# Performance work log

Measured on AMD Instinct MI355X. Metric: run time of the kernel, lower is better.

Reference implementation:

```python
import jax, jax.numpy as jnp
import numpy as np

N_OBJ = 4096      # n_objects (fixed node count; fc1 consumes flattened node features)
F_IN = 256        # in_feats
H = 256           # n_hidden
C = 128           # n_classes
NE = 8            # number of edge types
EPT = 131072      # edges per etype (avg in-degree 32)


def setup_inputs() -> dict:
    key = jax.random.key(0)
    ks = jax.random.split(key, 16)
    s = 0.02  # weight init scale
    inp = {
        "feat": jax.random.normal(ks[0], (N_OBJ, F_IN), dtype=jnp.float32),
        "edges": jax.random.randint(ks[1], (NE, 2, EPT), 0, N_OBJ, dtype=jnp.int64),
        # 3 hetero layers: layer0 (F_IN->H), layers 1,2 (H->H), each with per-etype Linear
        "W0": jax.random.normal(ks[2], (NE, H, F_IN), dtype=jnp.float32) * s,
        "b0": jnp.zeros((NE, H), dtype=jnp.float32),
        "W1": jax.random.normal(ks[3], (NE, H, H), dtype=jnp.float32) * s,
        "b1": jnp.zeros((NE, H), dtype=jnp.float32),
        "W2": jax.random.normal(ks[4], (NE, H, H), dtype=jnp.float32) * s,
        "b2": jnp.zeros((NE, H), dtype=jnp.float32),
        "fc1_w": jax.random.normal(ks[5], (H, N_OBJ * H), dtype=jnp.float32) * 0.002,
        "fc1_b": jnp.zeros((H,), dtype=jnp.float32),
        "fc2_w": jax.random.normal(ks[6], (C, H), dtype=jnp.float32) * s,
        "fc2_b": jnp.zeros((C,), dtype=jnp.float32),
    }
    return inp


def _hetero_layer(h, W, b, edges):
    # Per-etype linear: Wh[e] = h @ W[e].T + b[e]   -> [NE, N, H]
    Wh = jnp.einsum('nf,ehf->enh', h, W) + b[:, None, :]

    def per_etype(wh, src, dst):
        msg = wh[src]                                            # gather: [EPT, H]
        ssum = jax.ops.segment_sum(msg, dst, num_segments=N_OBJ)  # [N, H]
        deg = jax.ops.segment_sum(jnp.ones_like(dst, dtype=wh.dtype), dst,
                                  num_segments=N_OBJ)             # [N]
        return ssum / jnp.maximum(deg, 1.0)[:, None]              # mean reduce

    agg = jax.vmap(per_etype)(Wh, edges[:, 0], edges[:, 1])  # [NE, N, H]
    # multi_update_all cross-type aggregator 'sum', then activation (relu)
    return jax.nn.relu(agg.sum(axis=0))


def reference(feat, edges, W0, b0, W1, b1, W2, b2, fc1_w, fc1_b, fc2_w, fc2_b):
    h = _hetero_layer(feat, W0, b0, edges)
    h = _hetero_layer(h, W1, b1, edges)
    h = _hetero_layer(h, W2, b2, edges)
    flat = h.reshape(-1)                          # [N*H]
    z = jax.nn.relu(fc1_w @ flat + fc1_b)         # [H]
    out = jax.nn.sigmoid(fc2_w @ z + fc2_b)       # [C]
    return out
```

## Files before the change

### kernel.cpp

```cpp
#include <hip/hip_runtime.h>
#include <math.h>

#define N_OBJ 4096
#define F     256
#define NE    8
#define EPT   131072
#define KCAT  (NE * F)
#define C_OUT 128
#define FC1_K (N_OBJ * F)
#define CHUNK 32768
#define NCH   (FC1_K / CHUNK)
#define RPB   8

typedef __attribute__((ext_vector_type(8))) short s8v;
typedef __attribute__((ext_vector_type(4))) float f4v;

__device__ inline float bf2f(unsigned short u) {
    unsigned int x = ((unsigned int)u) << 16;
    return __builtin_bit_cast(float, x);
}
__device__ inline unsigned short f2bf(float f) {
    unsigned int x = __builtin_bit_cast(unsigned int, f);
    x += 0x7fff + ((x >> 16) & 1);
    return (unsigned short)(x >> 16);
}


__global__ __launch_bounds__(256) void k_count_deg(const int* __restrict__ edges,
                                                   int* __restrict__ deg) {
    int gid = blockIdx.x * 256 + threadIdx.x;
    int e = gid >> 17;
    int i = gid & (EPT - 1);
    int dst = edges[(e * 2 + 1) * EPT + i];
    atomicAdd(&deg[e * N_OBJ + dst], 1);
}

__global__ __launch_bounds__(256) void k_scan(const int* __restrict__ deg,
                                              int* __restrict__ rowptr,
                                              int* __restrict__ cursor,
                                              float* __restrict__ invdeg) {
    int e = blockIdx.x;
    int t = threadIdx.x;
    __shared__ int part[256];
    int local[16];
    int base = e * N_OBJ + t * 16;
    int s = 0;
#pragma unroll
    for (int i = 0; i < 16; ++i) { local[i] = deg[base + i]; s += local[i]; }
    part[t] = s;
    __syncthreads();
    for (int off = 1; off < 256; off <<= 1) {
        int v = (t >= off) ? part[t - off] : 0;
        __syncthreads();
        part[t] += v;
        __syncthreads();
    }
    int run = part[t] - s;
#pragma unroll
    for (int i = 0; i < 16; ++i) {
        rowptr[base + i] = run;
        cursor[base + i] = run;
        invdeg[base + i] = 1.0f / fmaxf((float)local[i], 1.0f);
        run += local[i];
    }
}

__global__ __launch_bounds__(256) void k_fill(const int* __restrict__ edges,
                                              int* __restrict__ cursor,
                                              int* __restrict__ col) {
    int gid = blockIdx.x * 256 + threadIdx.x;
    int e = gid >> 17;
    int i = gid & (EPT - 1);
    int src = edges[(e * 2 + 0) * EPT + i];
    int dst = edges[(e * 2 + 1) * EPT + i];
    int pos = atomicAdd(&cursor[e * N_OBJ + dst], 1);
    col[e * EPT + pos] = src;
}

__global__ __launch_bounds__(256) void k_bmask(const int* __restrict__ deg,
                                               unsigned int* __restrict__ bmask) {
    int n = blockIdx.x * 256 + threadIdx.x;
    unsigned int m = 0;
#pragma unroll
    for (int e = 0; e < NE; ++e) m |= (deg[e * N_OBJ + n] > 0) ? (1u << e) : 0u;
    bmask[n] = m;
}

__global__ __launch_bounds__(256) void k_cvt(const float* __restrict__ s,
                                             unsigned short* __restrict__ d, int n4) {
    int i = blockIdx.x * 256 + threadIdx.x;
    if (i < n4) {
        float4 v = ((const float4*)s)[i];
        ushort4 o;
        o.x = f2bf(v.x); o.y = f2bf(v.y); o.z = f2bf(v.z); o.w = f2bf(v.w);
        ((ushort4*)d)[i] = o;
    }
}

__global__ __launch_bounds__(256) void k_aggregate(const unsigned short* __restrict__ h_in,
                                                   const int* __restrict__ rowptr,
                                                   const int* __restrict__ deg,
                                                   const int* __restrict__ col,
                                                   const float* __restrict__ invdeg,
                                                   unsigned short* __restrict__ ah) {
    int wid = blockIdx.x * 4 + (threadIdx.x >> 6);
    int lane = threadIdx.x & 63;
    int e = wid >> 12;
    int n = wid & (N_OBJ - 1);
    int beg = rowptr[wid];
    int cnt = deg[wid];
    const int* cl = col + e * EPT + beg;
    const ushort4* h4 = (const ushort4*)h_in;
    float a0 = 0.f, a1 = 0.f, a2 = 0.f, a3 = 0.f;
    int k = 0;
    for (; k + 8 <= cnt; k += 8) {
        int s0 = cl[k],     s1 = cl[k + 1], s2 = cl[k + 2], s3 = cl[k + 3];
        int s4 = cl[k + 4], s5 = cl[k + 5], s6 = cl[k + 6], s7 = cl[k + 7];
        ushort4 v0 = h4[s0 * 64 + lane];
        ushort4 v1 = h4[s1 * 64 + lane];
        ushort4 v2 = h4[s2 * 64 + lane];
        ushort4 v3 = h4[s3 * 64 + lane];
        ushort4 v4 = h4[s4 * 64 + lane];
        ushort4 v5 = h4[s5 * 64 + lane];
        ushort4 v6 = h4[s6 * 64 + lane];
        ushort4 v7 = h4[s7 * 64 + lane];
        a0 += bf2f(v0.x) + bf2f(v1.x) + bf2f(v2.x) + bf2f(v3.x)
            + bf2f(v4.x) + bf2f(v5.x) + bf2f(v6.x) + bf2f(v7.x);
        a1 += bf2f(v0.y) + bf2f(v1.y) + bf2f(v2.y) + bf2f(v3.y)
            + bf2f(v4.y) + bf2f(v5.y) + bf2f(v6.y) + bf2f(v7.y);
        a2 += bf2f(v0.z) + bf2f(v1.z) + bf2f(v2.z) + bf2f(v3.z)
            + bf2f(v4.z) + bf2f(v5.z) + bf2f(v6.z) + bf2f(v7.z);
        a3 += bf2f(v0.w) + bf2f(v1.w) + bf2f(v2.w) + bf2f(v3.w)
            + bf2f(v4.w) + bf2f(v5.w) + bf2f(v6.w) + bf2f(v7.w);
    }
    for (; k < cnt; ++k) {
        ushort4 v = h4[cl[k] * 64 + lane];
        a0 += bf2f(v.x); a1 += bf2f(v.y); a2 += bf2f(v.z); a3 += bf2f(v.w);
    }
    float sc = invdeg[wid];
    ushort4 o;
    o.x = f2bf(a0 * sc); o.y = f2bf(a1 * sc); o.z = f2bf(a2 * sc); o.w = f2bf(a3 * sc);
    ((ushort4*)ah)[n * (KCAT / 4) + e * (F / 4) + lane] = o;
}

template <int OUTBF>
__global__ __launch_bounds__(256) void k_gemm(const unsigned short* __restrict__ A,
                                              const unsigned short* __restrict__ Wb,
                                              const float* __restrict__ bias,
                                              const unsigned int* __restrict__ bmask,
                                              void* __restrict__ Cout) {
    __shared__ short As[64][40];
    __shared__ short Bs[64][40];
    int m0 = blockIdx.x * 64, n0 = blockIdx.y * 64;
    int t = threadIdx.x;
    int wave = t >> 6, lane = t & 63;
    int srow = t >> 2, sseg = t & 3;
    int r = lane & 15, g = lane >> 4;
    f4v acc[4];
#pragma unroll
    for (int i = 0; i < 4; ++i) acc[i] = (f4v){0.f, 0.f, 0.f, 0.f};
    const short* Ap = (const short*)A;
    const short* Wp = (const short*)Wb;
    for (int k0 = 0; k0 < KCAT; k0 += 32) {
        int e = k0 >> 8, f0 = k0 & 255;
        s8v va = *(const s8v*)(Ap + (size_t)(m0 + srow) * KCAT + k0 + sseg * 8);
        s8v vb = *(const s8v*)(Wp + (size_t)e * F * F + (size_t)(n0 + srow) * F + f0 + sseg * 8);
        __syncthreads();
        *(s8v*)&As[srow][sseg * 8] = va;
        *(s8v*)&Bs[srow][sseg * 8] = vb;
        __syncthreads();
        s8v bfrag = *(const s8v*)&Bs[wave * 16 + r][g * 8];
#pragma unroll
        for (int mf = 0; mf < 4; ++mf) {
            s8v afrag = *(const s8v*)&As[mf * 16 + r][g * 8];
            acc[mf] = __builtin_amdgcn_mfma_f32_16x16x32_bf16(afrag, bfrag, acc[mf], 0, 0, 0);
        }
    }
    int coln = n0 + wave * 16 + r;
    float bcol[NE];
#pragma unroll
    for (int e = 0; e < NE; ++e) bcol[e] = bias[e * F + coln];
#pragma unroll
    for (int mf = 0; mf < 4; ++mf) {
#pragma unroll
        for (int reg = 0; reg < 4; ++reg) {
            int m = m0 + mf * 16 + g * 4 + reg;
            unsigned int msk = bmask[m];
            float v = acc[mf][reg];
#pragma unroll
            for (int e = 0; e < NE; ++e)
                if ((msk >> e) & 1) v += bcol[e];
            v = fmaxf(v, 0.f);
            if (OUTBF) ((unsigned short*)Cout)[(size_t)m * F + coln] = f2bf(v);
            else       ((float*)Cout)[(size_t)m * F + coln] = v;
        }
    }
}

__global__ __launch_bounds__(256) void k_fc1(const float* __restrict__ Wf,
                                             const float* __restrict__ flat,
                                             float* __restrict__ zpart) {
    int c = blockIdx.x;
    int jg = blockIdx.y;
    int t = threadIdx.x;
    const float4* fp = (const float4*)(flat + (size_t)c * CHUNK);
    size_t base = (size_t)(jg * RPB) * FC1_K + (size_t)c * CHUNK;
    float acc[RPB] = {};
#pragma unroll 2
    for (int it = 0; it < CHUNK / 4 / 256; ++it) {
        int q = it * 256 + t;
        float4 x4 = fp[q];
#pragma unroll
        for (int rr = 0; rr < RPB; ++rr) {
            float4 w4 = *(const float4*)(Wf + base + (size_t)rr * FC1_K + (size_t)q * 4);
            acc[rr] = fmaf(w4.x, x4.x,
                      fmaf(w4.y, x4.y,
                      fmaf(w4.z, x4.z,
                      fmaf(w4.w, x4.w, acc[rr]))));
        }
    }
    __shared__ float red[4][RPB];
    int lane = t & 63, wv = t >> 6;
#pragma unroll
    for (int rr = 0; rr < RPB; ++rr) {
        float s = acc[rr];
#pragma unroll
        for (int off = 32; off > 0; off >>= 1) s += __shfl_down(s, off, 64);
        if (lane == 0) red[wv][rr] = s;
    }
    __syncthreads();
    if (t < RPB) {
        float s = red[0][t] + red[1][t] + red[2][t] + red[3][t];
        zpart[c * 256 + jg * RPB + t] = s;
    }
}

__global__ __launch_bounds__(256) void k_final(const float* __restrict__ zpart,
                                               const float* __restrict__ fc1_b,
                                               const float* __restrict__ fc2_w,
                                               const float* __restrict__ fc2_b,
                                               float* __restrict__ out) {
    __shared__ float z[256];
    int t = threadIdx.x;
    float s = fc1_b[t];
#pragma unroll
    for (int c = 0; c < NCH; ++c) s += zpart[c * 256 + t];
    z[t] = fmaxf(s, 0.0f);
    __syncthreads();
    if (t < C_OUT) {
        float acc = fc2_b[t];
        for (int k = 0; k < 256; ++k) acc = fmaf(fc2_w[t * 256 + k], z[k], acc);
        out[t] = 1.0f / (1.0f + expf(-acc));
    }
}

extern "C" void kernel_launch(void* const* d_in, const int* in_sizes, int n_in,
                              void* d_out, int out_size, void* d_ws, size_t ws_size,
                              hipStream_t stream) {
    const float* feat  = (const float*)d_in[0];
    const int*   edges = (const int*)d_in[1];
    const float* W0    = (const float*)d_in[2];
    const float* b0    = (const float*)d_in[3];
    const float* W1    = (const float*)d_in[4];
    const float* b1    = (const float*)d_in[5];
    const float* W2    = (const float*)d_in[6];
    const float* b2    = (const float*)d_in[7];
    const float* fc1_w = (const float*)d_in[8];
    const float* fc1_b = (const float*)d_in[9];
    const float* fc2_w = (const float*)d_in[10];
    const float* fc2_b = (const float*)d_in[11];
    float* out = (float*)d_out;

    char* ws = (char*)d_ws;
    size_t off = 0;
    auto alloc = [&](size_t bytes) {
        void* p = ws + off;
        off = (off + bytes + 255) & ~(size_t)255;
        return p;
    };
    int*            deg    = (int*)            alloc(NE * N_OBJ * 4);
    int*            rowptr = (int*)            alloc(NE * N_OBJ * 4);
    int*            cursor = (int*)            alloc(NE * N_OBJ * 4);
    float*          invdeg = (float*)          alloc(NE * N_OBJ * 4);
    int*            col    = (int*)            alloc(NE * EPT * 4);
    unsigned int*   bmask  = (unsigned int*)   alloc(N_OBJ * 4);
    float*          zpart  = (float*)          alloc(NCH * 256 * 4);
    unsigned short* Wb0    = (unsigned short*) alloc((size_t)NE * F * F * 2);
    unsigned short* Wb1    = (unsigned short*) alloc((size_t)NE * F * F * 2);
    unsigned short* Wb2    = (unsigned short*) alloc((size_t)NE * F * F * 2);
    unsigned short* featb  = (unsigned short*) alloc((size_t)N_OBJ * F * 2);
    unsigned short* h_ba   = (unsigned short*) alloc((size_t)N_OBJ * F * 2);
    unsigned short* h_bb   = (unsigned short*) alloc((size_t)N_OBJ * F * 2);
    float*          h_f32  = (float*)          alloc((size_t)N_OBJ * F * 4);
    unsigned short* ah     = (unsigned short*) alloc((size_t)N_OBJ * KCAT * 2);
    (void)ws_size; (void)in_sizes; (void)n_in; (void)out_size;

    hipMemsetAsync(deg, 0, NE * N_OBJ * 4, stream);
    k_count_deg<<<NE * EPT / 256, 256, 0, stream>>>(edges, deg);
    k_scan<<<NE, 256, 0, stream>>>(deg, rowptr, cursor, invdeg);
    k_fill<<<NE * EPT / 256, 256, 0, stream>>>(edges, cursor, col);
    k_bmask<<<N_OBJ / 256, 256, 0, stream>>>(deg, bmask);
    k_cvt<<<512, 256, 0, stream>>>(W0, Wb0, NE * F * F / 4);
    k_cvt<<<512, 256, 0, stream>>>(W1, Wb1, NE * F * F / 4);
    k_cvt<<<512, 256, 0, stream>>>(W2, Wb2, NE * F * F / 4);
    k_cvt<<<1024, 256, 0, stream>>>(feat, featb, N_OBJ * F / 4);

    dim3 ggrid(N_OBJ / 64, F / 64);
    int agrid = NE * N_OBJ / 4;

    k_aggregate<<<agrid, 256, 0, stream>>>(featb, rowptr, deg, col, invdeg, ah);
    k_gemm<1><<<ggrid, 256, 0, stream>>>(ah, Wb0, b0, bmask, h_ba);
    k_aggregate<<<agrid, 256, 0, stream>>>(h_ba, rowptr, deg, col, invdeg, ah);
    k_gemm<1><<<ggrid, 256, 0, stream>>>(ah, Wb1, b1, bmask, h_bb);
    k_aggregate<<<agrid, 256, 0, stream>>>(h_bb, rowptr, deg, col, invdeg, ah);
    k_gemm<0><<<ggrid, 256, 0, stream>>>(ah, Wb2, b2, bmask, h_f32);

    dim3 fgrid(NCH, 256 / RPB);
    k_fc1<<<fgrid, 256, 0, stream>>>(fc1_w, h_f32, zpart);
    k_final<<<1, 256, 0, stream>>>(zpart, fc1_b, fc2_w, fc2_b, out);
}
```

Before: 522.9 us.

## Retile GEMM to 32x64 blocks, restructure fc1 per-row, merge conversion kernels

After: 522.2 us. Within noise of the previous version (-0.1%).

```diff
diff --git a/kernel.cpp b/kernel.cpp
--- a/kernel.cpp
+++ b/kernel.cpp
@@ -8,9 +8,6 @@
 #define KCAT  (NE * F)
 #define C_OUT 128
 #define FC1_K (N_OBJ * F)
-#define CHUNK 32768
-#define NCH   (FC1_K / CHUNK)
-#define RPB   8
 
 typedef __attribute__((ext_vector_type(8))) short s8v;
 typedef __attribute__((ext_vector_type(4))) float f4v;
@@ -86,15 +83,28 @@
     bmask[n] = m;
 }
 
-__global__ __launch_bounds__(256) void k_cvt(const float* __restrict__ s,
-                                             unsigned short* __restrict__ d, int n4) {
+#define WQ4 (NE * F * F / 4)
+#define FQ4 (N_OBJ * F / 4)
+__global__ __launch_bounds__(256) void k_cvt_all(const float* __restrict__ W0,
+                                                 const float* __restrict__ W1,
+                                                 const float* __restrict__ W2,
+                                                 const float* __restrict__ feat,
+                                                 unsigned short* __restrict__ Wb0,
+                                                 unsigned short* __restrict__ Wb1,
+                                                 unsigned short* __restrict__ Wb2,
+                                                 unsigned short* __restrict__ featb) {
     int i = blockIdx.x * 256 + threadIdx.x;
-    if (i < n4) {
-        float4 v = ((const float4*)s)[i];
-        ushort4 o;
-        o.x = f2bf(v.x); o.y = f2bf(v.y); o.z = f2bf(v.z); o.w = f2bf(v.w);
-        ((ushort4*)d)[i] = o;
-    }
+    const float* s;
+    unsigned short* d;
+    int j;
+    if (i < WQ4)            { s = W0;   d = Wb0;   j = i; }
+    else if (i < 2 * WQ4)   { s = W1;   d = Wb1;   j = i - WQ4; }
+    else if (i < 3 * WQ4)   { s = W2;   d = Wb2;   j = i - 2 * WQ4; }
+    else                    { s = feat; d = featb; j = i - 3 * WQ4; }
+    float4 v = ((const float4*)s)[j];
+    ushort4 o;
+    o.x = f2bf(v.x); o.y = f2bf(v.y); o.z = f2bf(v.z); o.w = f2bf(v.w);
+    ((ushort4*)d)[j] = o;
 }
 
 __global__ __launch_bounds__(256) void k_aggregate(const unsigned short* __restrict__ h_in,
@@ -144,55 +154,66 @@
 }
 
 template <int OUTBF>
-__global__ __launch_bounds__(256) void k_gemm(const unsigned short* __restrict__ A,
+__global__ __launch_bounds__(128) void k_gemm(const unsigned short* __restrict__ A,
                                               const unsigned short* __restrict__ Wb,
                                               const float* __restrict__ bias,
                                               const unsigned int* __restrict__ bmask,
                                               void* __restrict__ Cout) {
-    __shared__ short As[64][40];
+    __shared__ short As[32][40];
     __shared__ short Bs[64][40];
-    int m0 = blockIdx.x * 64, n0 = blockIdx.y * 64;
+    int m0 = blockIdx.x * 32, n0 = blockIdx.y * 64;
     int t = threadIdx.x;
     int wave = t >> 6, lane = t & 63;
-    int srow = t >> 2, sseg = t & 3;
     int r = lane & 15, g = lane >> 4;
-    f4v acc[4];
-#pragma unroll
-    for (int i = 0; i < 4; ++i) acc[i] = (f4v){0.f, 0.f, 0.f, 0.f};
+    int arow = t >> 2, aseg = t & 3;
+    int brow = t >> 1, bseg = (t & 1) * 2;
+    f4v acc[2][2];
+#pragma unroll
+    for (int i = 0; i < 2; ++i)
+#pragma unroll
+        for (int j = 0; j < 2; ++j) acc[i][j] = (f4v){0.f, 0.f, 0.f, 0.f};
     const short* Ap = (const short*)A;
     const short* Wp = (const short*)Wb;
     for (int k0 = 0; k0 < KCAT; k0 += 32) {
         int e = k0 >> 8, f0 = k0 & 255;
-        s8v va = *(const s8v*)(Ap + (size_t)(m0 + srow) * KCAT + k0 + sseg * 8);
-        s8v vb = *(const s8v*)(Wp + (size_t)e * F * F + (size_t)(n0 + srow) * F + f0 + sseg * 8);
+        s8v va = *(const s8v*)(Ap + (size_t)(m0 + arow) * KCAT + k0 + aseg * 8);
+        const short* wbase = Wp + (size_t)e * F * F + (size_t)(n0 + brow) * F + f0;
+        s8v vb0 = *(const s8v*)(wbase + bseg * 8);
+        s8v vb1 = *(const s8v*)(wbase + bseg * 8 + 8);
         __syncthreads();
-        *(s8v*)&As[srow][sseg * 8] = va;
-        *(s8v*)&Bs[srow][sseg * 8] = vb;
+        *(s8v*)&As[arow][aseg * 8] = va;
+        *(s8v*)&Bs[brow][bseg * 8] = vb0;
+        *(s8v*)&Bs[brow][bseg * 8 + 8] = vb1;
         __syncthreads();
-        s8v bfrag = *(const s8v*)&Bs[wave * 16 + r][g * 8];
-#pragma unroll
-        for (int mf = 0; mf < 4; ++mf) {
-            s8v afrag = *(const s8v*)&As[mf * 16 + r][g * 8];
-            acc[mf] = __builtin_amdgcn_mfma_f32_16x16x32_bf16(afrag, bfrag, acc[mf], 0, 0, 0);
+        s8v bf0 = *(const s8v*)&Bs[wave * 32 + r][g * 8];
+        s8v bf1 = *(const s8v*)&Bs[wave * 32 + 16 + r][g * 8];
+#pragma unroll
+        for (int m = 0; m < 2; ++m) {
+            s8v af = *(const s8v*)&As[m * 16 + r][g * 8];
+            acc[m][0] = __builtin_amdgcn_mfma_f32_16x16x32_bf16(af, bf0, acc[m][0], 0, 0, 0);
+            acc[m][1] = __builtin_amdgcn_mfma_f32_16x16x32_bf16(af, bf1, acc[m][1], 0, 0, 0);
         }
     }
-    int coln = n0 + wave * 16 + r;
-    float bcol[NE];
-#pragma unroll
-    for (int e = 0; e < NE; ++e) bcol[e] = bias[e * F + coln];
-#pragma unroll
-    for (int mf = 0; mf < 4; ++mf) {
-#pragma unroll
-        for (int reg = 0; reg < 4; ++reg) {
-            int m = m0 + mf * 16 + g * 4 + reg;
-            unsigned int msk = bmask[m];
-            float v = acc[mf][reg];
-#pragma unroll
-            for (int e = 0; e < NE; ++e)
-                if ((msk >> e) & 1) v += bcol[e];
-            v = fmaxf(v, 0.f);
-            if (OUTBF) ((unsigned short*)Cout)[(size_t)m * F + coln] = f2bf(v);
-            else       ((float*)Cout)[(size_t)m * F + coln] = v;
+#pragma unroll
+    for (int nn = 0; nn < 2; ++nn) {
+        int coln = n0 + wave * 32 + nn * 16 + r;
+        float bcol[NE];
+#pragma unroll
+        for (int e = 0; e < NE; ++e) bcol[e] = bias[e * F + coln];
+#pragma unroll
+        for (int m = 0; m < 2; ++m) {
+#pragma unroll
+            for (int reg = 0; reg < 4; ++reg) {
+                int mm = m0 + m * 16 + g * 4 + reg;
+                unsigned int msk = bmask[mm];
+                float v = acc[m][nn][reg];
+#pragma unroll
+                for (int e = 0; e < NE; ++e)
+                    if ((msk >> e) & 1) v += bcol[e];
+                v = fmaxf(v, 0.f);
+                if (OUTBF) ((unsigned short*)Cout)[(size_t)mm * F + coln] = f2bf(v);
+                else       ((float*)Cout)[(size_t)mm * F + coln] = v;
+            }
         }
     }
 }
@@ -201,38 +222,27 @@
                                              const float* __restrict__ flat,
                                              float* __restrict__ zpart) {
     int c = blockIdx.x;
-    int jg = blockIdx.y;
+    int j = blockIdx.y;
     int t = threadIdx.x;
-    const float4* fp = (const float4*)(flat + (size_t)c * CHUNK);
-    size_t base = (size_t)(jg * RPB) * FC1_K + (size_t)c * CHUNK;
-    float acc[RPB] = {};
-#pragma unroll 2
-    for (int it = 0; it < CHUNK / 4 / 256; ++it) {
+    const float4* wp = (const float4*)(Wf + (size_t)j * FC1_K + (size_t)c * 65536);
+    const float4* fp = (const float4*)(flat + (size_t)c * 65536);
+    float s = 0.0f;
+#pragma unroll 8
+    for (int it = 0; it < 64; ++it) {
         int q = it * 256 + t;
+        float4 w4 = wp[q];
         float4 x4 = fp[q];
-#pragma unroll
-        for (int rr = 0; rr < RPB; ++rr) {
-            float4 w4 = *(const float4*)(Wf + base + (size_t)rr * FC1_K + (size_t)q * 4);
-            acc[rr] = fmaf(w4.x, x4.x,
-                      fmaf(w4.y, x4.y,
-                      fmaf(w4.z, x4.z,
-                      fmaf(w4.w, x4.w, acc[rr]))));
-        }
-    }
-    __shared__ float red[4][RPB];
-    int lane = t & 63, wv = t >> 6;
-#pragma unroll
-    for (int rr = 0; rr < RPB; ++rr) {
-        float s = acc[rr];
-#pragma unroll
-        for (int off = 32; off > 0; off >>= 1) s += __shfl_down(s, off, 64);
-        if (lane == 0) red[wv][rr] = s;
-    }
+        s = fmaf(w4.x, x4.x, s);
+        s = fmaf(w4.y, x4.y, s);
+        s = fmaf(w4.z, x4.z, s);
+        s = fmaf(w4.w, x4.w, s);
+    }
+#pragma unroll
+    for (int off = 32; off > 0; off >>= 1) s += __shfl_down(s, off, 64);
+    __shared__ float red[4];
+    if ((t & 63) == 0) red[t >> 6] = s;
     __syncthreads();
-    if (t < RPB) {
-        float s = red[0][t] + red[1][t] + red[2][t] + red[3][t];
-        zpart[c * 256 + jg * RPB + t] = s;
-    }
+    if (t == 0) zpart[c * 256 + j] = red[0] + red[1] + red[2] + red[3];
 }
 
 __global__ __launch_bounds__(256) void k_final(const float* __restrict__ zpart,
@@ -244,7 +254,7 @@
     int t = threadIdx.x;
     float s = fc1_b[t];
 #pragma unroll
-    for (int c = 0; c < NCH; ++c) s += zpart[c * 256 + t];
+    for (int c = 0; c < 16; ++c) s += zpart[c * 256 + t];
     z[t] = fmaxf(s, 0.0f);
     __syncthreads();
     if (t < C_OUT) {
@@ -284,7 +294,7 @@
     float*          invdeg = (float*)          alloc(NE * N_OBJ * 4);
     int*            col    = (int*)            alloc(NE * EPT * 4);
     unsigned int*   bmask  = (unsigned int*)   alloc(N_OBJ * 4);
-    float*          zpart  = (float*)          alloc(NCH * 256 * 4);
+    float*          zpart  = (float*)          alloc(16 * 256 * 4);
     unsigned short* Wb0    = (unsigned short*) alloc((size_t)NE * F * F * 2);
     unsigned short* Wb1    = (unsigned short*) alloc((size_t)NE * F * F * 2);
     unsigned short* Wb2    = (unsigned short*) alloc((size_t)NE * F * F * 2);
@@ -300,22 +310,20 @@
     k_scan<<<NE, 256, 0, stream>>>(deg, rowptr, cursor, invdeg);
     k_fill<<<NE * EPT / 256, 256, 0, stream>>>(edges, cursor, col);
     k_bmask<<<N_OBJ / 256, 256, 0, stream>>>(deg, bmask);
-    k_cvt<<<512, 256, 0, stream>>>(W0, Wb0, NE * F * F / 4);
-    k_cvt<<<512, 256, 0, stream>>>(W1, Wb1, NE * F * F / 4);
-    k_cvt<<<512, 256, 0, stream>>>(W2, Wb2, NE * F * F / 4);
-    k_cvt<<<1024, 256, 0, stream>>>(feat, featb, N_OBJ * F / 4);
-
-    dim3 ggrid(N_OBJ / 64, F / 64);
+    k_cvt_all<<<(3 * WQ4 + FQ4) / 256, 256, 0, stream>>>(W0, W1, W2, feat,
+                                                         Wb0, Wb1, Wb2, featb);
+
+    dim3 ggrid(N_OBJ / 32, F / 64);
     int agrid = NE * N_OBJ / 4;
 
     k_aggregate<<<agrid, 256, 0, stream>>>(featb, rowptr, deg, col, invdeg, ah);
-    k_gemm<1><<<ggrid, 256, 0, stream>>>(ah, Wb0, b0, bmask, h_ba);
+    k_gemm<1><<<ggrid, 128, 0, stream>>>(ah, Wb0, b0, bmask, h_ba);
     k_aggregate<<<agrid, 256, 0, stream>>>(h_ba, rowptr, deg, col, invdeg, ah);
-    k_gemm<1><<<ggrid, 256, 0, stream>>>(ah, Wb1, b1, bmask, h_bb);
+    k_gemm<1><<<ggrid, 128, 0, stream>>>(ah, Wb1, b1, bmask, h_bb);
     k_aggregate<<<agrid, 256, 0, stream>>>(h_bb, rowptr, deg, col, invdeg, ah);
-    k_gemm<0><<<ggrid, 256, 0, stream>>>(ah, Wb2, b2, bmask, h_f32);
-
-    dim3 fgrid(NCH, 256 / RPB);
+    k_gemm<0><<<ggrid, 128, 0, stream>>>(ah, Wb2, b2, bmask, h_f32);
+
+    dim3 fgrid(16, 256);
     k_fc1<<<fgrid, 256, 0, stream>>>(fc1_w, h_f32, zpart);
     k_final<<<1, 256, 0, stream>>>(zpart, fc1_b, fc2_w, fc2_b, out);
 }
```
